# Performance work log

Hardware: AMD Instinct MI355X
Metric: run time of the kernel (lower is better)

## Reference

```python
import jax, jax.numpy as jnp
import numpy as np
from jax import lax

NUM_NEURONS = 144
NUM_E = 115  # int(144 * 0.8)
NEURONS_PER_CELL = 16
TAU = 2.0
V_TH = 1.0

# action -> (dx, dy) -> grid cell -> neuron slice; precomputed 5x144 current table
_ACTION_TO_POS = {0: (1, 0), 1: (0, -1), 2: (-1, 0), 3: (0, 1), 4: (0, 0)}

def _build_action_table():
    tab = np.zeros((5, NUM_NEURONS), dtype=np.float32)
    for a, (dx, dy) in _ACTION_TO_POS.items():
        x, y = 1 + dx, 1 + dy
        if 0 <= x < 3 and 0 <= y < 3:
            cell = y * 3 + x
            tab[a, cell * NEURONS_PER_CELL:(cell + 1) * NEURONS_PER_CELL] = 5.0
    return jnp.asarray(tab)

_EI_MASK = jnp.concatenate([jnp.ones(NUM_E, jnp.float32), -jnp.ones(NUM_NEURONS - NUM_E, jnp.float32)])


def setup_inputs() -> dict:
    key = jax.random.key(0)
    k1, k2, k3, k4 = jax.random.split(key, 4)
    B, NB = 16384, 8
    actions = jax.random.randint(k1, (B,), 0, 5)
    neighbor_E_spikes = (jax.random.uniform(k2, (B, NB, NUM_E)) < 0.2).astype(jnp.float32)
    W_rec = jax.random.normal(k3, (NUM_NEURONS, NUM_NEURONS), jnp.float32) * 0.01
    mask = jax.random.uniform(jax.random.fold_in(k3, 1), (NUM_NEURONS, NUM_NEURONS)) >= 0.9
    W_rec = W_rec * mask.astype(jnp.float32)
    W_inh = jax.random.normal(k4, (NUM_NEURONS, NUM_E), jnp.float32) * 0.1
    return {"actions": actions, "neighbor_E_spikes": neighbor_E_spikes,
            "W_rec": W_rec, "W_inh": W_inh, "num_ticks": 30}


def reference(actions, neighbor_E_spikes, W_rec, W_inh, num_ticks):
    B = actions.shape[0]
    input_current = _build_action_table()[actions]  # [B, 144]
    # neighbor loop == sum over neighbors, constant across ticks
    inhibition = jnp.einsum('bne,oe->bo', neighbor_E_spikes, W_inh)  # [B, 144]
    const_drive = 0.5 * input_current - 0.5 * inhibition

    def step(carry, _):
        v, acc = carry
        rec = (acc @ W_rec.T) * _EI_MASK          # recurrent input with Dale mask
        x = const_drive + 0.3 * rec
        v = v + (x - v) / TAU                      # LIF charge (decay_input=True, v_reset=0)
        s = (v >= V_TH).astype(v.dtype)            # spike
        v = v * (1.0 - s)                          # hard reset to 0
        return (v, acc + s), None

    init = (jnp.zeros((B, NUM_NEURONS), jnp.float32), jnp.zeros((B, NUM_NEURONS), jnp.float32))
    (_, acc), _ = lax.scan(step, init, None, length=num_ticks)
    return acc[:, :NUM_E]
```

## Files before the change

### kernel.cpp

```cpp
#include <hip/hip_runtime.h>
#include <string.h>


#define NN 144
#define NE 115
#define NB 64
#define WAVES 16
#define RPW 9
#define THREADS 1024

#define CSR_BYTE_OFF 4096

__device__ __forceinline__ float u2f(unsigned u) {
    float f; memcpy(&f, &u, 4); return f;
}

__global__ void prep_kernel(const float* __restrict__ W_rec,
                            int* __restrict__ wsI, char* __restrict__ wsB) {
    __shared__ int cnt[NN];
    __shared__ int rp[NN + 1];
    int t = threadIdx.x;

    if (t < NN) {
        int c = 0;
        for (int j = 0; j < NN; ++j) c += (W_rec[t * NN + j] != 0.0f);
        cnt[t] = c;
    }
    __syncthreads();
    if (t == 0) {
        int s = 0; rp[0] = 0;
        for (int o = 0; o < NN; ++o) { s += (cnt[o] + 3) & ~3; rp[o + 1] = s; }
    }
    __syncthreads();
    if (t <= NN) wsI[t] = rp[t];
    char* base = wsB + CSR_BYTE_OFF;
    if (t < NN) {
        int p = rp[t];
        for (int j = 0; j < NN; ++j) {
            float w = W_rec[t * NN + j];
            if (w != 0.0f) {
                *(int*)(base + 8 * (size_t)p)     = j;
                *(float*)(base + 8 * (size_t)p + 4) = w;
                ++p;
            }
        }
        for (; p < rp[t + 1]; ++p) {
            *(int*)(base + 8 * (size_t)p)       = 0;
            *(float*)(base + 8 * (size_t)p + 4) = 0.0f;
        }
    }
    if (t < 16) {
        int p = rp[NN] + t;
        *(int*)(base + 8 * (size_t)p)       = 0;
        *(float*)(base + 8 * (size_t)p + 4) = 0.0f;
    }
}

__global__ __launch_bounds__(THREADS) void snn_kernel(
        const int*   __restrict__ actions,
        const float* __restrict__ spk,
        const float* __restrict__ W_inh,
        const int*   __restrict__ wsI,
        const uint4* __restrict__ csrQ,
        const int*   __restrict__ nt_ptr,
        float*       __restrict__ out,
        int B) {
    __shared__ float accF[2][NN * NB];
    __shared__ int   rpL[NN + 1];

    float* nbF = (float*)&accF[1][0];

    const int t    = threadIdx.x;
    const int lane = t & 63;
    const int wid  = t >> 6;
    const int b0   = blockIdx.x * NB;
    const int b    = b0 + lane;
    const int ticks = *nt_ptr;
    const int R0   = wid * RPW;

    int vz;
    asm volatile("v_mov_b32 %0, 0" : "=v"(vz));

    if (t <= NN) rpL[t] = wsI[t];

    for (int p = t; p < NB * NE; p += THREADS) {
        int bb = p / NE;
        int e  = p - bb * NE;
        float s = 0.0f;
        if (b0 + bb < B) {
            const float* sp = spk + ((size_t)(b0 + bb) * 8) * NE + e;
            #pragma unroll
            for (int n = 0; n < 8; ++n) s += sp[n * NE];
        }
        nbF[e * (NB + 1) + bb] = s;
    }
    for (int i = t; i < NN * NB; i += THREADS) accF[0][i] = 0.0f;
    __syncthreads();

    const int R0s = __builtin_amdgcn_readfirstlane(R0);
    double drv[RPW];
    {
        int a = (b < B) ? actions[b] : 4;
        int cell = (a == 0) ? 5 : (a == 1) ? 1 : (a == 2) ? 3 : (a == 3) ? 7 : 4;
        int cs = cell * 16;
        #pragma unroll
        for (int r = 0; r < RPW; ++r) {
            double inh = 0.0;
            for (int e = 0; e < NE; ++e)
                inh += (double)nbF[e * (NB + 1) + lane]
                     * (double)W_inh[(R0s + r) * NE + e];
            int o = R0 + r;
            double ic = (o >= cs && o < cs + 16) ? 5.0 : 0.0;
            drv[r] = 0.5 * ic - 0.5 * inh;
        }
    }

    int sk0[RPW], sk1[RPW];
    #pragma unroll
    for (int r = 0; r < RPW; ++r) {
        sk0[r] = __builtin_amdgcn_readfirstlane(rpL[R0 + r]);
        sk1[r] = __builtin_amdgcn_readfirstlane(rpL[R0 + r + 1]);
    }
    const int K00 = sk0[0];

    double v[RPW];
    float  accv[RPW];
    #pragma unroll
    for (int r = 0; r < RPW; ++r) { v[r] = 0.0; accv[r] = 0.0f; }

    for (int tk = 0; tk < ticks; ++tk) {
        __syncthreads();
        const float* __restrict__ Rb = accF[tk & 1];
        float*       __restrict__ Wb = accF[(tk & 1) ^ 1];

        int q0 = (K00 >> 1) + vz;
        uint4 A0 = csrQ[q0],     A1 = csrQ[q0 + 1];
        uint4 B0 = csrQ[q0 + 2], B1 = csrQ[q0 + 3];

        #pragma unroll
        for (int r = 0; r < RPW; ++r) {
            const int o = R0 + r;
            double rec = 0.0;
            for (int k = sk0[r]; k < sk1[r]; k += 4) {
                int qn = (k >> 1) + vz;
                uint4 C0 = csrQ[qn + 4], C1 = csrQ[qn + 5];
                float a0 = Rb[((int)A0.x << 6) + lane];
                float a1 = Rb[((int)A0.z << 6) + lane];
                float a2 = Rb[((int)A1.x << 6) + lane];
                float a3 = Rb[((int)A1.z << 6) + lane];
                rec += (double)u2f(A0.y) * (double)a0;
                rec += (double)u2f(A0.w) * (double)a1;
                rec += (double)u2f(A1.y) * (double)a2;
                rec += (double)u2f(A1.w) * (double)a3;
                A0 = B0; A1 = B1; B0 = C0; B1 = C1;
            }
            double x = drv[r] + 0.3 * ((o < NE) ? rec : -rec);
            double vv = v[r];
            vv += (x - vv) * 0.5;
            double s = (vv >= 1.0) ? 1.0 : 0.0;
            vv *= (1.0 - s);
            v[r] = vv;
            accv[r] += (float)s;
            Wb[(o << 6) + lane] = accv[r];
        }
    }

    if (b < B) {
        #pragma unroll
        for (int r = 0; r < RPW; ++r) {
            int o = R0 + r;
            if (o < NE) out[(size_t)b * NE + o] = accv[r];
        }
    }
}

extern "C" void kernel_launch(void* const* d_in, const int* in_sizes, int n_in,
                              void* d_out, int out_size, void* d_ws, size_t ws_size,
                              hipStream_t stream) {
    const int*   actions = (const int*)  d_in[0];
    const float* spk     = (const float*)d_in[1];
    const float* W_rec   = (const float*)d_in[2];
    const float* W_inh   = (const float*)d_in[3];
    const int*   nt      = (const int*)  d_in[4];
    float* out = (float*)d_out;
    int B = in_sizes[0];

    int*  wsI = (int*)d_ws;
    char* wsB = (char*)d_ws;
    const uint4* csrQ = (const uint4*)(wsB + CSR_BYTE_OFF);

    prep_kernel<<<1, 256, 0, stream>>>(W_rec, wsI, wsB);
    int nblocks = (B + NB - 1) / NB;
    snn_kernel<<<nblocks, THREADS, 0, stream>>>(actions, spk, W_inh, wsI, csrQ,
                                                nt, out, B);
}
```

Measured before the change: 377.7 us.

## Sort rows by nnz and pack quads so each lane handles four batches via float4 LDS

Prep now sorts recurrent-weight rows by nonzero count. It packs 128 rows into quads of similar length and puts the 16 leftover rows in a solo CSR, then assigns each wave two quads (balanced front and back) plus one solo row. In the tick loop a 16-lane subgroup owns one row of a quad, and each lane reads four batch elements at once with float4 LDS loads, which cuts LDS instructions and evens out per-wave work. The cost is a more complex prep kernel, padding inside quads, and more double-precision registers per lane.

Result: slower. 395.5 us (+4.7%).

```diff
diff --git a/kernel.cpp b/kernel.cpp
--- a/kernel.cpp
+++ b/kernel.cpp
@@ -5,21 +5,25 @@
 #define NN 144
 #define NE 115
 #define NB 64
-#define WAVES 16
-#define RPW 9
 #define THREADS 1024
 
-#define CSR_BYTE_OFF 4096
+#define QUAD_BASE 4096
+#define SOLO_BASE 53248
+#define REGION_END 61440
 
 __device__ __forceinline__ float u2f(unsigned u) {
     float f; memcpy(&f, &u, 4); return f;
 }
 
 __global__ void prep_kernel(const float* __restrict__ W_rec,
-                            int* __restrict__ wsI, char* __restrict__ wsB) {
+                            int* __restrict__ meta, char* __restrict__ wsB) {
     __shared__ int cnt[NN];
-    __shared__ int rp[NN + 1];
-    int t = threadIdx.x;
+    __shared__ int sorted[NN];
+    __shared__ int kqS[32], ksS[16], qOS[32], sOS[16];
+    const int t = threadIdx.x;
+
+    for (int i = t; i < (REGION_END - QUAD_BASE) / 4; i += 256)
+        ((int*)(wsB + QUAD_BASE))[i] = 0;
 
     if (t < NN) {
         int c = 0;
@@ -27,61 +31,148 @@
         cnt[t] = c;
     }
     __syncthreads();
+    if (t < NN) {
+        int ct = cnt[t], r = 0;
+        for (int j = 0; j < NN; ++j) {
+            int cj = cnt[j];
+            r += (cj > ct) || (cj == ct && j < t);
+        }
+        sorted[r] = t;
+    }
+    __syncthreads();
     if (t == 0) {
-        int s = 0; rp[0] = 0;
-        for (int o = 0; o < NN; ++o) { s += (cnt[o] + 3) & ~3; rp[o + 1] = s; }
-    }
-    __syncthreads();
-    if (t <= NN) wsI[t] = rp[t];
-    char* base = wsB + CSR_BYTE_OFF;
-    if (t < NN) {
-        int p = rp[t];
+        int off = 0;
+        for (int q = 0; q < 32; ++q) {
+            int mx = cnt[sorted[4 * q]];
+            int kq = ((mx < 1 ? 1 : mx) + 3) & ~3;
+            kqS[q] = kq; qOS[q] = off; off += kq * 32;
+        }
+        int so = 0;
+        for (int s = 0; s < 16; ++s) {
+            int c = cnt[sorted[128 + s]];
+            int ks = ((c < 1 ? 1 : c) + 3) & ~3;
+            ksS[s] = ks; sOS[s] = so; so += ks * 8;
+        }
+    }
+    __syncthreads();
+    if (t < 128) {
+        int q = t >> 2, i = t & 3, R = sorted[4 * q + i];
+        char* base = wsB + QUAD_BASE + qOS[q] + i * 8;
+        int k = 0;
         for (int j = 0; j < NN; ++j) {
-            float w = W_rec[t * NN + j];
+            float w = W_rec[R * NN + j];
             if (w != 0.0f) {
-                *(int*)(base + 8 * (size_t)p)     = j;
-                *(float*)(base + 8 * (size_t)p + 4) = w;
-                ++p;
+                *(unsigned*)(base + (size_t)k * 32)    = (unsigned)j * 256u;
+                *(float*)(base + (size_t)k * 32 + 4)   = w;
+                ++k;
             }
         }
-        for (; p < rp[t + 1]; ++p) {
-            *(int*)(base + 8 * (size_t)p)       = 0;
-            *(float*)(base + 8 * (size_t)p + 4) = 0.0f;
+    } else if (t < 144) {
+        int s = t - 128, R = sorted[128 + s];
+        char* base = wsB + SOLO_BASE + sOS[s];
+        int k = 0;
+        for (int j = 0; j < NN; ++j) {
+            float w = W_rec[R * NN + j];
+            if (w != 0.0f) {
+                *(unsigned*)(base + (size_t)k * 8)   = (unsigned)j * 256u;
+                *(float*)(base + (size_t)k * 8 + 4)  = w;
+                ++k;
+            }
         }
     }
     if (t < 16) {
-        int p = rp[NN] + t;
-        *(int*)(base + 8 * (size_t)p)       = 0;
-        *(float*)(base + 8 * (size_t)p + 4) = 0.0f;
-    }
-}
+        int w = t;
+        int* m = meta + w * 16;
+        m[0] = qOS[w];      m[1] = kqS[w];
+        m[2] = qOS[31 - w]; m[3] = kqS[31 - w];
+        for (int i = 0; i < 4; ++i) m[4 + i] = sorted[4 * w + i];
+        for (int i = 0; i < 4; ++i) m[8 + i] = sorted[4 * (31 - w) + i];
+        m[12] = sOS[w]; m[13] = ksS[w]; m[14] = sorted[128 + w];
+    }
+}
+
+#define QF(S)                                                           \
+    {                                                                   \
+        float4 a4 = *(const float4*)(ldsB + ((S).x + lroQ));            \
+        double wq = (double)u2f((S).y);                                 \
+        RQ0 += wq * (double)a4.x;                                       \
+        RQ1 += wq * (double)a4.y;                                       \
+        RQ2 += wq * (double)a4.z;                                       \
+        RQ3 += wq * (double)a4.w;                                       \
+    }
+
+#define QUAD_SEC(QOFF, QK, ROW, DRV, VQ, AQ)                            \
+    {                                                                   \
+        const uint2* p = (const uint2*)(wsQ + (QOFF)) + sub;            \
+        uint2 S0 = p[0], S1 = p[4], S2 = p[8], S3 = p[12];              \
+        double RQ0 = 0.0, RQ1 = 0.0, RQ2 = 0.0, RQ3 = 0.0;              \
+        for (int k = 0; k + 4 <= (QK); k += 4) {                        \
+            QF(S0); S0 = p[16];                                         \
+            QF(S1); S1 = p[20];                                         \
+            QF(S2); S2 = p[24];                                         \
+            QF(S3); S3 = p[28];                                         \
+            p += 16;                                                    \
+        }                                                               \
+        const bool exc = (ROW) < NE;                                    \
+        double recs[4] = {RQ0, RQ1, RQ2, RQ3};                          \
+        _Pragma("unroll")                                               \
+        for (int j = 0; j < 4; ++j) {                                   \
+            double rec = recs[j];                                       \
+            double x = (DRV)[j] + 0.3 * (exc ? rec : -rec);             \
+            double vv = (VQ)[j];                                        \
+            vv += (x - vv) * 0.5;                                       \
+            double sd = (vv >= 1.0) ? 1.0 : 0.0;                        \
+            vv *= (1.0 - sd);                                           \
+            (VQ)[j] = vv;                                               \
+            (AQ)[j] += (float)sd;                                       \
+        }                                                               \
+        float4 st; st.x=(AQ)[0]; st.y=(AQ)[1]; st.z=(AQ)[2]; st.w=(AQ)[3]; \
+        *(float4*)(WbB + (unsigned)(ROW) * 256u + ((lane & 15) * 16)) = st; \
+    }
+
+#define GS4(S0, S1)                                                     \
+    {                                                                   \
+        float a0 = *(const float*)(ldsB + ((S0).x + lroS));             \
+        float a1 = *(const float*)(ldsB + ((S0).z + lroS));             \
+        float a2 = *(const float*)(ldsB + ((S1).x + lroS));             \
+        float a3 = *(const float*)(ldsB + ((S1).z + lroS));             \
+        recS += (double)u2f((S0).y) * (double)a0;                       \
+        recS += (double)u2f((S0).w) * (double)a1;                       \
+        recS += (double)u2f((S1).y) * (double)a2;                       \
+        recS += (double)u2f((S1).w) * (double)a3;                       \
+    }
 
 __global__ __launch_bounds__(THREADS) void snn_kernel(
         const int*   __restrict__ actions,
         const float* __restrict__ spk,
         const float* __restrict__ W_inh,
-        const int*   __restrict__ wsI,
-        const uint4* __restrict__ csrQ,
+        const int*   __restrict__ meta,
+        const char*  __restrict__ wsB,
         const int*   __restrict__ nt_ptr,
         float*       __restrict__ out,
         int B) {
-    __shared__ float accF[2][NN * NB];
-    __shared__ int   rpL[NN + 1];
-
-    float* nbF = (float*)&accF[1][0];
+    __shared__ __align__(16) float accF[2][NN * NB];
+
+    const char* ldsB = (const char*)&accF[0][0];
+    char*       nbB  = (char*)&accF[1][0];
+    const char* wsQ  = wsB + QUAD_BASE;
+    const char* wsS  = wsB + SOLO_BASE;
 
     const int t    = threadIdx.x;
     const int lane = t & 63;
     const int wid  = t >> 6;
+    const int sub  = lane >> 4;
     const int b0   = blockIdx.x * NB;
-    const int b    = b0 + lane;
     const int ticks = *nt_ptr;
-    const int R0   = wid * RPW;
+
+    const int* mw = meta + wid * 16;
+    const int qO0 = mw[0], qk0 = mw[1], qO1 = mw[2], qk1 = mw[3];
+    const int r0  = mw[4 + sub];
+    const int r1  = mw[8 + sub];
+    const int sO  = mw[12], sk = mw[13], srow = mw[14];
 
     int vz;
     asm volatile("v_mov_b32 %0, 0" : "=v"(vz));
-
-    if (t <= NN) rpL[t] = wsI[t];
 
     for (int p = t; p < NB * NE; p += THREADS) {
         int bb = p / NE;
@@ -92,86 +183,88 @@
             #pragma unroll
             for (int n = 0; n < 8; ++n) s += sp[n * NE];
         }
-        nbF[e * (NB + 1) + bb] = s;
+        *(float*)(nbB + (size_t)e * 256 + (size_t)bb * 4) = s;
     }
     for (int i = t; i < NN * NB; i += THREADS) accF[0][i] = 0.0f;
     __syncthreads();
 
-    const int R0s = __builtin_amdgcn_readfirstlane(R0);
-    double drv[RPW];
+    double inh0[4] = {0,0,0,0}, inh1[4] = {0,0,0,0}, inhS = 0.0;
+    for (int e = 0; e < NE; ++e) {
+        float4 nb4 = *(const float4*)(nbB + e * 256 + (lane & 15) * 16);
+        float  nbs = *(const float*)(nbB + e * 256 + lane * 4);
+        double w0 = (double)W_inh[r0 * NE + e];
+        double w1 = (double)W_inh[r1 * NE + e];
+        double w2 = (double)W_inh[srow * NE + e];
+        inh0[0] += (double)nb4.x * w0; inh0[1] += (double)nb4.y * w0;
+        inh0[2] += (double)nb4.z * w0; inh0[3] += (double)nb4.w * w0;
+        inh1[0] += (double)nb4.x * w1; inh1[1] += (double)nb4.y * w1;
+        inh1[2] += (double)nb4.z * w1; inh1[3] += (double)nb4.w * w1;
+        inhS += (double)nbs * w2;
+    }
+    const int bqb = b0 + 4 * (lane & 15);
+    double drv0[4], drv1[4], drvS;
     {
-        int a = (b < B) ? actions[b] : 4;
-        int cell = (a == 0) ? 5 : (a == 1) ? 1 : (a == 2) ? 3 : (a == 3) ? 7 : 4;
-        int cs = cell * 16;
         #pragma unroll
-        for (int r = 0; r < RPW; ++r) {
-            double inh = 0.0;
-            for (int e = 0; e < NE; ++e)
-                inh += (double)nbF[e * (NB + 1) + lane]
-                     * (double)W_inh[(R0s + r) * NE + e];
-            int o = R0 + r;
-            double ic = (o >= cs && o < cs + 16) ? 5.0 : 0.0;
-            drv[r] = 0.5 * ic - 0.5 * inh;
-        }
-    }
-
-    int sk0[RPW], sk1[RPW];
-    #pragma unroll
-    for (int r = 0; r < RPW; ++r) {
-        sk0[r] = __builtin_amdgcn_readfirstlane(rpL[R0 + r]);
-        sk1[r] = __builtin_amdgcn_readfirstlane(rpL[R0 + r + 1]);
-    }
-    const int K00 = sk0[0];
-
-    double v[RPW];
-    float  accv[RPW];
-    #pragma unroll
-    for (int r = 0; r < RPW; ++r) { v[r] = 0.0; accv[r] = 0.0f; }
+        for (int j = 0; j < 4; ++j) {
+            int bi = bqb + j; if (bi >= B) bi = B - 1;
+            int a = actions[bi];
+            int cs = ((a == 0) ? 5 : (a == 1) ? 1 : (a == 2) ? 3 : (a == 3) ? 7 : 4) * 16;
+            double ic0 = (r0 >= cs && r0 < cs + 16) ? 5.0 : 0.0;
+            double ic1 = (r1 >= cs && r1 < cs + 16) ? 5.0 : 0.0;
+            drv0[j] = 0.5 * ic0 - 0.5 * inh0[j];
+            drv1[j] = 0.5 * ic1 - 0.5 * inh1[j];
+        }
+        int bi = b0 + lane; if (bi >= B) bi = B - 1;
+        int a = actions[bi];
+        int cs = ((a == 0) ? 5 : (a == 1) ? 1 : (a == 2) ? 3 : (a == 3) ? 7 : 4) * 16;
+        double icS = (srow >= cs && srow < cs + 16) ? 5.0 : 0.0;
+        drvS = 0.5 * icS - 0.5 * inhS;
+    }
+
+    double vq0[4] = {0,0,0,0}, vq1[4] = {0,0,0,0}, vS = 0.0;
+    float  aq0[4] = {0,0,0,0}, aq1[4] = {0,0,0,0}, aS = 0.0f;
 
     for (int tk = 0; tk < ticks; ++tk) {
         __syncthreads();
-        const float* __restrict__ Rb = accF[tk & 1];
-        float*       __restrict__ Wb = accF[(tk & 1) ^ 1];
-
-        int q0 = (K00 >> 1) + vz;
-        uint4 A0 = csrQ[q0],     A1 = csrQ[q0 + 1];
-        uint4 B0 = csrQ[q0 + 2], B1 = csrQ[q0 + 3];
-
-        #pragma unroll
-        for (int r = 0; r < RPW; ++r) {
-            const int o = R0 + r;
-            double rec = 0.0;
-            for (int k = sk0[r]; k < sk1[r]; k += 4) {
-                int qn = (k >> 1) + vz;
-                uint4 C0 = csrQ[qn + 4], C1 = csrQ[qn + 5];
-                float a0 = Rb[((int)A0.x << 6) + lane];
-                float a1 = Rb[((int)A0.z << 6) + lane];
-                float a2 = Rb[((int)A1.x << 6) + lane];
-                float a3 = Rb[((int)A1.z << 6) + lane];
-                rec += (double)u2f(A0.y) * (double)a0;
-                rec += (double)u2f(A0.w) * (double)a1;
-                rec += (double)u2f(A1.y) * (double)a2;
-                rec += (double)u2f(A1.w) * (double)a3;
-                A0 = B0; A1 = B1; B0 = C0; B1 = C1;
+        const unsigned rbOff = (tk & 1) ? 36864u : 0u;
+        const unsigned lroQ  = (unsigned)((lane & 15) * 16) + rbOff;
+        const unsigned lroS  = (unsigned)(lane * 4) + rbOff;
+        char* WbB = (char*)ldsB + ((tk & 1) ? 0u : 36864u);
+
+        QUAD_SEC(qO0, qk0, r0, drv0, vq0, aq0);
+        QUAD_SEC(qO1, qk1, r1, drv1, vq1, aq1);
+
+        {
+            const uint4* ps = (const uint4*)(wsS + sO) + vz;
+            uint4 A0 = ps[0], A1 = ps[1], B0q = ps[2], B1q = ps[3];
+            double recS = 0.0;
+            int k = 0;
+            for (; k + 8 <= sk; k += 8) {
+                GS4(A0, A1);   A0 = ps[4]; A1 = ps[5];
+                GS4(B0q, B1q); B0q = ps[6]; B1q = ps[7];
+                ps += 4;
             }
-            double x = drv[r] + 0.3 * ((o < NE) ? rec : -rec);
-            double vv = v[r];
+            if (k < sk) { GS4(A0, A1); }
+            double x = drvS + 0.3 * ((srow < NE) ? recS : -recS);
+            double vv = vS;
             vv += (x - vv) * 0.5;
-            double s = (vv >= 1.0) ? 1.0 : 0.0;
-            vv *= (1.0 - s);
-            v[r] = vv;
-            accv[r] += (float)s;
-            Wb[(o << 6) + lane] = accv[r];
-        }
-    }
-
-    if (b < B) {
-        #pragma unroll
-        for (int r = 0; r < RPW; ++r) {
-            int o = R0 + r;
-            if (o < NE) out[(size_t)b * NE + o] = accv[r];
-        }
-    }
+            double sd = (vv >= 1.0) ? 1.0 : 0.0;
+            vv *= (1.0 - sd);
+            vS = vv;
+            aS += (float)sd;
+            *(float*)(WbB + (unsigned)srow * 256u + lane * 4) = aS;
+        }
+    }
+
+    #pragma unroll
+    for (int j = 0; j < 4; ++j) {
+        int bi = bqb + j;
+        if (bi < B) {
+            if (r0 < NE) out[(size_t)bi * NE + r0] = aq0[j];
+            if (r1 < NE) out[(size_t)bi * NE + r1] = aq1[j];
+        }
+    }
+    if (b0 + lane < B && srow < NE) out[(size_t)(b0 + lane) * NE + srow] = aS;
 }
 
 extern "C" void kernel_launch(void* const* d_in, const int* in_sizes, int n_in,
@@ -185,12 +278,11 @@
     float* out = (float*)d_out;
     int B = in_sizes[0];
 
-    int*  wsI = (int*)d_ws;
-    char* wsB = (char*)d_ws;
-    const uint4* csrQ = (const uint4*)(wsB + CSR_BYTE_OFF);
-
-    prep_kernel<<<1, 256, 0, stream>>>(W_rec, wsI, wsB);
+    int*  meta = (int*)d_ws;
+    char* wsB  = (char*)d_ws;
+
+    prep_kernel<<<1, 256, 0, stream>>>(W_rec, meta, wsB);
     int nblocks = (B + NB - 1) / NB;
-    snn_kernel<<<nblocks, THREADS, 0, stream>>>(actions, spk, W_inh, wsI, csrQ,
+    snn_kernel<<<nblocks, THREADS, 0, stream>>>(actions, spk, W_inh, meta, wsB,
                                                 nt, out, B);
 }
```
